# Kernel optimization log

Measured on AMD Instinct MI355X. Metric: run time of the kernel, lower is better.

The kernel has to match this reference:

```python
import jax, jax.numpy as jnp
import numpy as np

H = 1024
E = 8
TOP_K = 2
B, S = 4, 2048


def setup_inputs() -> dict:
    key = jax.random.key(0)
    ks = jax.random.split(key, 8)
    scale = 0.02
    return {
        "x": jax.random.normal(ks[0], (B, S, H), dtype=jnp.float32),
        "router_w": jax.random.normal(ks[1], (H, E), dtype=jnp.float32) * scale,
        "router_b": jnp.zeros((E,), dtype=jnp.float32),
        "w1": jax.random.normal(ks[2], (E, H, 4 * H), dtype=jnp.float32) * scale,
        "b1": jnp.zeros((E, 4 * H), dtype=jnp.float32),
        "w2": jax.random.normal(ks[3], (E, 4 * H, H), dtype=jnp.float32) * scale,
        "b2": jnp.zeros((E, H), dtype=jnp.float32),
    }


def reference(x, router_w, router_b, w1, b1, w2, b2):
    b, s, h = x.shape
    n_exp = w1.shape[0]
    x_flat = x.reshape(-1, h)  # [T, H]
    T = x_flat.shape[0]

    # Router: softmax then top-k, renormalize top-k probs (matches torch code).
    logits = x_flat @ router_w + router_b            # [T, E]
    probs = jax.nn.softmax(logits, axis=-1)
    top_values, top_indices = jax.lax.top_k(probs, TOP_K)  # [T, k]
    top_values = top_values / jnp.sum(top_values, axis=-1, keepdims=True)

    # Per-token combine weight for each expert (0 if token not routed there).
    combine = jnp.zeros((T, n_exp), dtype=x.dtype)
    combine = combine.at[jnp.arange(T)[:, None], top_indices].add(top_values)  # [T, E]

    # Loop over the small fixed expert set; masked combine weights zero out
    # contributions from unrouted tokens, matching the gather/scatter original.
    out = jnp.zeros_like(x_flat)
    for e in range(n_exp):
        hmid = jax.nn.gelu(x_flat @ w1[e] + b1[e], approximate=False)  # [T, 4H]
        y = hmid @ w2[e] + b2[e]                                       # [T, H]
        out = out + combine[:, e:e + 1] * y
    return out.reshape(b, s, h)
```

## Files before the change

kernel.cpp:

```cpp
#include <hip/hip_runtime.h>
#include <hip/hip_bf16.h>
#include <math.h>

#define TT 8192
#define HD 1024
#define FHD 4096
#define NE 8
#define NTMAX 136

typedef short s16x8 __attribute__((ext_vector_type(8)));
typedef float f32x4 __attribute__((ext_vector_type(4)));
using bf16 = __hip_bfloat16;
typedef unsigned int u32;

#define OFF_COUNTS 0
#define OFF_DONE   32
#define OFF_CURSOR 64
#define OFF_OFFS   128
#define OFF_E0     256
#define OFF_E1     (OFF_E0 + 4*TT)
#define OFF_W0     (OFF_E1 + 4*TT)
#define OFF_W1     (OFF_W0 + 4*TT)
#define OFF_S0     (OFF_W1 + 4*TT)
#define OFF_S1     (OFF_S0 + 4*TT)
#define OFF_TID    (OFF_S1 + 4*TT)
#define OFF_TW     (OFF_TID + 8*TT)
#define OFF_TMR    (OFF_TW + 8*TT)
#define OFF_TME    (OFF_TMR + 4*144)
#define OFF_TMN    (OFF_TME + 4*144)
#define OFF_XBF    (OFF_TMN + 64)
#define OFF_W1T    (OFF_XBF + 2*TT*HD)
#define OFF_W2T    (OFF_W1T + 2*NE*HD*FHD)
#define OFF_HMID   (OFF_W2T + 2*NE*HD*FHD)
#define OFF_YS     (OFF_HMID + (size_t)2*(2*TT)*FHD)

__device__ __forceinline__ void gload_lds16(const void* g, void* l) {
    __builtin_amdgcn_global_load_lds(
        (const __attribute__((address_space(1))) u32*)g,
        (__attribute__((address_space(3))) u32*)l, 16, 0, 0);
}

__global__ __launch_bounds__(256) void prep_kernel(
        const float* __restrict__ x, const float* __restrict__ rw, const float* __restrict__ rb,
        const float* __restrict__ w1, const float* __restrict__ w2,
        bf16* __restrict__ xbf, bf16* __restrict__ w1t, bf16* __restrict__ w2t,
        int* __restrict__ e0a, int* __restrict__ e1a,
        float* __restrict__ w0a, float* __restrict__ w1a,
        int* __restrict__ counts, int* __restrict__ done,
        int* __restrict__ offs, int* __restrict__ cursor,
        int* __restrict__ tmr, int* __restrict__ tme, int* __restrict__ tmn) {
    __shared__ float tile[64][65];
    __shared__ bf16 btile[64][264];
    int bid = blockIdx.x;
    int tid = threadIdx.x;
    if (bid < 4096) {
        const float* in; bf16* out; int R, C, rem;
        if (bid < 2048) { in = w1; out = w1t; R = HD;  C = FHD; rem = bid; }
        else            { in = w2; out = w2t; R = FHD; C = HD;  rem = bid - 2048; }
        int kch = R >> 8;
        int nch = C >> 6;
        int per = kch * nch;
        int e = rem / per;
        int rem2 = rem % per;
        int kc = rem2 / nch, nc = rem2 % nch;
        int k0 = kc << 8, n0 = nc << 6;
        const float* ine = in + (size_t)e * R * C;
        bf16* oute = out + (size_t)e * R * C;
        for (int s = 0; s < 4; ++s) {
            int ks = k0 + s * 64;
#pragma unroll
            for (int i = 0; i < 4; ++i) {
                int lin = tid + i * 256;
                int r = lin >> 4, cg = lin & 15;
                float4 v = *reinterpret_cast<const float4*>(&ine[(size_t)(ks + r) * C + n0 + cg * 4]);
                tile[r][cg * 4 + 0] = v.x; tile[r][cg * 4 + 1] = v.y;
                tile[r][cg * 4 + 2] = v.z; tile[r][cg * 4 + 3] = v.w;
            }
            __syncthreads();
#pragma unroll
            for (int i = 0; i < 4; ++i) {
                int lin = tid + i * 256;
                int n = lin >> 4, kg = lin & 15;
                bf16 h[4];
                h[0] = __float2bfloat16(tile[kg * 4 + 0][n]);
                h[1] = __float2bfloat16(tile[kg * 4 + 1][n]);
                h[2] = __float2bfloat16(tile[kg * 4 + 2][n]);
                h[3] = __float2bfloat16(tile[kg * 4 + 3][n]);
                *reinterpret_cast<uint2*>(&btile[n][s * 64 + kg * 4]) = *reinterpret_cast<uint2*>(h);
            }
            __syncthreads();
        }
#pragma unroll
        for (int i = 0; i < 8; ++i) {
            int lin = tid + i * 256;
            int n = lin >> 5, kk = lin & 31;
            *reinterpret_cast<uint4*>(&oute[(size_t)(n0 + n) * R + k0 + kk * 8]) =
                *reinterpret_cast<const uint4*>(&btile[n][kk * 8]);
        }
        return;
    }
    int rbid = bid - 4096;
    int wid = tid >> 6, lane = tid & 63;
    int t = rbid * 4 + wid;
    const float* xp = x + (size_t)t * HD + lane * 16;
    float xv[16];
#pragma unroll
    for (int j = 0; j < 4; ++j) {
        float4 v = *reinterpret_cast<const float4*>(&xp[j * 4]);
        xv[4 * j] = v.x; xv[4 * j + 1] = v.y; xv[4 * j + 2] = v.z; xv[4 * j + 3] = v.w;
    }
    {
        bf16 hv[16];
#pragma unroll
        for (int j = 0; j < 16; ++j) hv[j] = __float2bfloat16(xv[j]);
        uint4* dst = reinterpret_cast<uint4*>(&xbf[(size_t)t * HD + lane * 16]);
        dst[0] = reinterpret_cast<uint4*>(hv)[0];
        dst[1] = reinterpret_cast<uint4*>(hv)[1];
    }
    float acc[8] = {0.f, 0.f, 0.f, 0.f, 0.f, 0.f, 0.f, 0.f};
    const float* rp = rw + (size_t)(lane * 16) * NE;
#pragma unroll
    for (int hh = 0; hh < 16; ++hh) {
        float4 r0 = *reinterpret_cast<const float4*>(&rp[hh * 8]);
        float4 r1 = *reinterpret_cast<const float4*>(&rp[hh * 8 + 4]);
        acc[0] += xv[hh] * r0.x; acc[1] += xv[hh] * r0.y;
        acc[2] += xv[hh] * r0.z; acc[3] += xv[hh] * r0.w;
        acc[4] += xv[hh] * r1.x; acc[5] += xv[hh] * r1.y;
        acc[6] += xv[hh] * r1.z; acc[7] += xv[hh] * r1.w;
    }
#pragma unroll
    for (int e = 0; e < 8; ++e) {
#pragma unroll
        for (int off = 32; off > 0; off >>= 1) acc[e] += __shfl_xor(acc[e], off, 64);
    }
    if (lane == 0) {
        float lg[8];
#pragma unroll
        for (int e = 0; e < 8; ++e) lg[e] = acc[e] + rb[e];
        int a = 0;
#pragma unroll
        for (int e = 1; e < 8; ++e) if (lg[e] > lg[a]) a = e;
        int b = (a == 0) ? 1 : 0;
#pragma unroll
        for (int e = 0; e < 8; ++e) if (e != a && e != b && lg[e] > lg[b]) b = e;
        float wa = 1.0f / (1.0f + expf(lg[b] - lg[a]));
        float wb = 1.0f / (1.0f + expf(lg[a] - lg[b]));
        e0a[t] = a; e1a[t] = b; w0a[t] = wa; w1a[t] = wb;
        atomicAdd(&counts[a], 1);
        atomicAdd(&counts[b], 1);
    }
    __syncthreads();
    __shared__ int lastFlag;
    if (tid == 0) {
        __threadfence();
        lastFlag = (atomicAdd(done, 1) == 2047) ? 1 : 0;
    }
    __syncthreads();
    if (!lastFlag) return;
    __threadfence();
    __shared__ int cbase[NE + 1], tbase[NE + 1];
    if (tid == 0) {
        int s = 0, ntt = 0;
        for (int e = 0; e < NE; ++e) {
            int c = atomicAdd(&counts[e], 0);
            cbase[e] = s; tbase[e] = ntt;
            s += c; ntt += (c + 127) >> 7;
        }
        cbase[NE] = s; tbase[NE] = ntt;
        tmn[0] = ntt;
        offs[NE] = s;
    }
    __syncthreads();
    if (tid < NE) { offs[tid] = cbase[tid]; cursor[tid] = cbase[tid]; }
    if (tid < NTMAX) {
        int ntt = tbase[NE];
        if (tid < ntt) {
            int e = 0;
            while (tbase[e + 1] <= tid) ++e;
            tmr[tid] = cbase[e] + ((tid - tbase[e]) << 7);
            tme[tid] = e;
        } else { tmr[tid] = 0; tme[tid] = 0; }
    }
}

__global__ __launch_bounds__(256) void scatter_kernel(const int* __restrict__ e0a, const int* __restrict__ e1a,
        const float* __restrict__ w0a, const float* __restrict__ w1a,
        int* __restrict__ cursor, int* __restrict__ tid_arr, float* __restrict__ tw_arr,
        int* __restrict__ slot0, int* __restrict__ slot1) {
    int t = blockIdx.x * 256 + threadIdx.x;
    int s0 = atomicAdd(&cursor[e0a[t]], 1);
    tid_arr[s0] = t; tw_arr[s0] = w0a[t]; slot0[t] = s0;
    int s1 = atomicAdd(&cursor[e1a[t]], 1);
    tid_arr[s1] = t; tw_arr[s1] = w1a[t]; slot1[t] = s1;
}

__global__ __launch_bounds__(256) void gemm1_kernel(const bf16* __restrict__ xbf, const bf16* __restrict__ w1t,
        const float* __restrict__ b1, const int* __restrict__ offs,
        const int* __restrict__ tid_arr, bf16* __restrict__ hmid,
        const int* __restrict__ tmr, const int* __restrict__ tme, const int* __restrict__ tmn) {
    __shared__ bf16 As[128 * 32];
    __shared__ bf16 Bs[128 * 32];
    __shared__ int toks[128];
    int nwg = gridDim.x;
    int orig = blockIdx.x;
    int wg = (orig & 7) * (nwg >> 3) + (orig >> 3);
    int nt = wg / NTMAX;
    int tidx = wg % NTMAX;
    if (tidx >= tmn[0]) return;
    int e = tme[tidx];
    int row0 = tmr[tidx];
    int s1 = offs[e + 1];
    int n0 = nt * 128;
    int tid = threadIdx.x;
    if (tid < 128) { int s = row0 + tid; toks[tid] = tid_arr[(s < s1) ? s : (s1 - 1)]; }
    __syncthreads();
    int lane = tid & 63, w = tid >> 6;
    int wrow = (w >> 1) * 64, wcol = (w & 1) * 64;
    int lr = lane & 15, lk = (lane >> 4) * 8;
    int srow = lane >> 2, seg = lane & 3;
    int tokA0 = toks[w * 32 + srow];
    int tokA1 = toks[w * 32 + 16 + srow];
    const bf16* w1e = w1t + (size_t)e * FHD * HD;
    const bf16* bsrc0 = w1e + (size_t)(n0 + w * 32 + srow) * HD + seg * 8;
    const bf16* bsrc1 = w1e + (size_t)(n0 + w * 32 + 16 + srow) * HD + seg * 8;
    const bf16* asrc0 = xbf + (size_t)tokA0 * HD + seg * 8;
    const bf16* asrc1 = xbf + (size_t)tokA1 * HD + seg * 8;
    bf16* aDst0 = &As[(w * 32) * 32];
    bf16* aDst1 = &As[(w * 32 + 16) * 32];
    bf16* bDst0 = &Bs[(w * 32) * 32];
    bf16* bDst1 = &Bs[(w * 32 + 16) * 32];
    f32x4 acc[4][4] = {};
    for (int k0 = 0; k0 < HD; k0 += 32) {
        gload_lds16(asrc0 + k0, aDst0);
        gload_lds16(asrc1 + k0, aDst1);
        gload_lds16(bsrc0 + k0, bDst0);
        gload_lds16(bsrc1 + k0, bDst1);
        __syncthreads();
        s16x8 aF[4], bF[4];
#pragma unroll
        for (int m = 0; m < 4; ++m) aF[m] = *reinterpret_cast<const s16x8*>(&As[(wrow + m * 16 + lr) * 32 + lk]);
#pragma unroll
        for (int n = 0; n < 4; ++n) bF[n] = *reinterpret_cast<const s16x8*>(&Bs[(wcol + n * 16 + lr) * 32 + lk]);
#pragma unroll
        for (int m = 0; m < 4; ++m)
#pragma unroll
            for (int n = 0; n < 4; ++n)
                acc[m][n] = __builtin_amdgcn_mfma_f32_16x16x32_bf16(aF[m], bF[n], acc[m][n], 0, 0, 0);
        __syncthreads();
    }
#pragma unroll
    for (int m = 0; m < 4; ++m) {
#pragma unroll
        for (int n = 0; n < 4; ++n) {
            int col = n0 + wcol + n * 16 + lr;
            float bv = b1[(size_t)e * FHD + col];
#pragma unroll
            for (int r = 0; r < 4; ++r) {
                int row = wrow + m * 16 + (lane >> 4) * 4 + r;
                int slot = row0 + row;
                if (slot < s1) {
                    float v2 = acc[m][n][r] + bv;
                    v2 = 0.5f * v2 * (1.0f + erff(v2 * 0.70710678118f));
                    hmid[(size_t)slot * FHD + col] = __float2bfloat16(v2);
                }
            }
        }
    }
}

__global__ __launch_bounds__(256) void gemm2_kernel(const bf16* __restrict__ hmid, const bf16* __restrict__ w2t,
        const float* __restrict__ b2, const int* __restrict__ offs, float* __restrict__ ys,
        const int* __restrict__ tmr, const int* __restrict__ tme, const int* __restrict__ tmn) {
    __shared__ bf16 As[128 * 32];
    __shared__ bf16 Bs[128 * 32];
    int nwg = gridDim.x;
    int orig = blockIdx.x;
    int wg = (orig & 7) * (nwg >> 3) + (orig >> 3);
    int nt = wg / NTMAX;
    int tidx = wg % NTMAX;
    if (tidx >= tmn[0]) return;
    int e = tme[tidx];
    int row0 = tmr[tidx];
    int s1 = offs[e + 1];
    int n0 = nt * 128;
    int tid = threadIdx.x;
    int lane = tid & 63, w = tid >> 6;
    int wrow = (w >> 1) * 64, wcol = (w & 1) * 64;
    int lr = lane & 15, lk = (lane >> 4) * 8;
    int srow = lane >> 2, seg = lane & 3;
    int ar0 = row0 + w * 32 + srow;      if (ar0 >= s1) ar0 = s1 - 1;
    int ar1 = row0 + w * 32 + 16 + srow; if (ar1 >= s1) ar1 = s1 - 1;
    const bf16* w2e = w2t + (size_t)e * HD * FHD;
    const bf16* bsrc0 = w2e + (size_t)(n0 + w * 32 + srow) * FHD + seg * 8;
    const bf16* bsrc1 = w2e + (size_t)(n0 + w * 32 + 16 + srow) * FHD + seg * 8;
    const bf16* asrc0 = hmid + (size_t)ar0 * FHD + seg * 8;
    const bf16* asrc1 = hmid + (size_t)ar1 * FHD + seg * 8;
    bf16* aDst0 = &As[(w * 32) * 32];
    bf16* aDst1 = &As[(w * 32 + 16) * 32];
    bf16* bDst0 = &Bs[(w * 32) * 32];
    bf16* bDst1 = &Bs[(w * 32 + 16) * 32];
    f32x4 acc[4][4] = {};
    for (int k0 = 0; k0 < FHD; k0 += 32) {
        gload_lds16(asrc0 + k0, aDst0);
        gload_lds16(asrc1 + k0, aDst1);
        gload_lds16(bsrc0 + k0, bDst0);
        gload_lds16(bsrc1 + k0, bDst1);
        __syncthreads();
        s16x8 aF[4], bF[4];
#pragma unroll
        for (int m = 0; m < 4; ++m) aF[m] = *reinterpret_cast<const s16x8*>(&As[(wrow + m * 16 + lr) * 32 + lk]);
#pragma unroll
        for (int n = 0; n < 4; ++n) bF[n] = *reinterpret_cast<const s16x8*>(&Bs[(wcol + n * 16 + lr) * 32 + lk]);
#pragma unroll
        for (int m = 0; m < 4; ++m)
#pragma unroll
            for (int n = 0; n < 4; ++n)
                acc[m][n] = __builtin_amdgcn_mfma_f32_16x16x32_bf16(aF[m], bF[n], acc[m][n], 0, 0, 0);
        __syncthreads();
    }
#pragma unroll
    for (int m = 0; m < 4; ++m) {
#pragma unroll
        for (int n = 0; n < 4; ++n) {
            int col = n0 + wcol + n * 16 + lr;
            float bv = b2[(size_t)e * HD + col];
#pragma unroll
            for (int r = 0; r < 4; ++r) {
                int row = wrow + m * 16 + (lane >> 4) * 4 + r;
                int slot = row0 + row;
                if (slot < s1) ys[(size_t)slot * HD + col] = acc[m][n][r] + bv;
            }
        }
    }
}

__global__ __launch_bounds__(256) void combine_kernel(const float* __restrict__ ys,
        const int* __restrict__ slot0, const int* __restrict__ slot1,
        const float* __restrict__ tw, float* __restrict__ out) {
    int t = blockIdx.x;
    int c = threadIdx.x * 4;
    int sa = slot0[t], sb = slot1[t];
    float wa = tw[sa], wb = tw[sb];
    float4 a = *reinterpret_cast<const float4*>(&ys[(size_t)sa * HD + c]);
    float4 b = *reinterpret_cast<const float4*>(&ys[(size_t)sb * HD + c]);
    float4 o;
    o.x = wa * a.x + wb * b.x; o.y = wa * a.y + wb * b.y;
    o.z = wa * a.z + wb * b.z; o.w = wa * a.w + wb * b.w;
    *reinterpret_cast<float4*>(&out[(size_t)t * HD + c]) = o;
}

extern "C" void kernel_launch(void* const* d_in, const int* in_sizes, int n_in,
                              void* d_out, int out_size, void* d_ws, size_t ws_size,
                              hipStream_t stream) {
    const float* x  = (const float*)d_in[0];
    const float* rw = (const float*)d_in[1];
    const float* rb = (const float*)d_in[2];
    const float* w1 = (const float*)d_in[3];
    const float* b1 = (const float*)d_in[4];
    const float* w2 = (const float*)d_in[5];
    const float* b2 = (const float*)d_in[6];
    float* out = (float*)d_out;
    char* ws = (char*)d_ws;

    int*   counts  = (int*)(ws + OFF_COUNTS);
    int*   done    = (int*)(ws + OFF_DONE);
    int*   cursor  = (int*)(ws + OFF_CURSOR);
    int*   offs    = (int*)(ws + OFF_OFFS);
    int*   e0a     = (int*)(ws + OFF_E0);
    int*   e1a     = (int*)(ws + OFF_E1);
    float* w0a     = (float*)(ws + OFF_W0);
    float* w1a     = (float*)(ws + OFF_W1);
    int*   slot0   = (int*)(ws + OFF_S0);
    int*   slot1   = (int*)(ws + OFF_S1);
    int*   tid_arr = (int*)(ws + OFF_TID);
    float* tw_arr  = (float*)(ws + OFF_TW);
    int*   tmr     = (int*)(ws + OFF_TMR);
    int*   tme     = (int*)(ws + OFF_TME);
    int*   tmn     = (int*)(ws + OFF_TMN);
    bf16*  xbf     = (bf16*)(ws + OFF_XBF);
    bf16*  w1t     = (bf16*)(ws + OFF_W1T);
    bf16*  w2t     = (bf16*)(ws + OFF_W2T);
    bf16*  hmid    = (bf16*)(ws + OFF_HMID);
    float* ys      = (float*)(ws + OFF_YS);

    hipMemsetAsync(counts, 0, 64, stream);

    prep_kernel<<<6144, 256, 0, stream>>>(x, rw, rb, w1, w2, xbf, w1t, w2t,
        e0a, e1a, w0a, w1a, counts, done, offs, cursor, tmr, tme, tmn);
    scatter_kernel<<<TT / 256, 256, 0, stream>>>(e0a, e1a, w0a, w1a, cursor,
        tid_arr, tw_arr, slot0, slot1);
    gemm1_kernel<<<(FHD / 128) * NTMAX, 256, 0, stream>>>(xbf, w1t, b1, offs, tid_arr, hmid, tmr, tme, tmn);
    gemm2_kernel<<<(HD / 128) * NTMAX, 256, 0, stream>>>(hmid, w2t, b2, offs, ys, tmr, tme, tmn);
    combine_kernel<<<TT, 256, 0, stream>>>(ys, slot0, slot1, tw_arr, out);
}
```

Measured before the change: 917.2 us.

## Overlap w2 transpose with gemm1 by fusing both into one launch

The w2 fp32-to-bf16 transpose moves out of the prep kernel into the same grid as the first expert GEMM. Low block indices do the transpose panels and the rest run gemm1 tiles, so the bandwidth-bound conversion can overlap with the compute-bound GEMM. The fused kernel uses a shared 50KB LDS buffer for both roles, which may lower gemm1 occupancy compared with its original smaller footprint. Block dispatch order sends the transpose blocks first, which may delay the start of the GEMM work.

```diff
diff --git a/kernel.cpp b/kernel.cpp
--- a/kernel.cpp
+++ b/kernel.cpp
@@ -7,6 +7,7 @@
 #define FHD 4096
 #define NE 8
 #define NTMAX 136
+#define NWG1 4352
 
 typedef short s16x8 __attribute__((ext_vector_type(8)));
 typedef float f32x4 __attribute__((ext_vector_type(4)));
@@ -40,66 +41,67 @@
         (__attribute__((address_space(3))) u32*)l, 16, 0, 0);
 }
 
-__global__ __launch_bounds__(256) void prep_kernel(
+__device__ __forceinline__ void transpose_panel(const float* __restrict__ in,
+        bf16* __restrict__ out, int R, int C, int rem, int tid, char* smem) {
+    float (*tile)[65]  = reinterpret_cast<float(*)[65]>(smem);
+    bf16  (*btile)[264] = reinterpret_cast<bf16(*)[264]>(smem + 16640);
+    int kch = R >> 8, nch = C >> 6;
+    int per = kch * nch;
+    int e = rem / per;
+    int rem2 = rem % per;
+    int kc = rem2 / nch, nc = rem2 % nch;
+    int k0 = kc << 8, n0 = nc << 6;
+    const float* ine = in + (size_t)e * R * C;
+    bf16* oute = out + (size_t)e * R * C;
+    for (int s = 0; s < 4; ++s) {
+        int ks = k0 + s * 64;
+#pragma unroll
+        for (int i = 0; i < 4; ++i) {
+            int lin = tid + i * 256;
+            int r = lin >> 4, cg = lin & 15;
+            float4 v = *reinterpret_cast<const float4*>(&ine[(size_t)(ks + r) * C + n0 + cg * 4]);
+            tile[r][cg * 4 + 0] = v.x; tile[r][cg * 4 + 1] = v.y;
+            tile[r][cg * 4 + 2] = v.z; tile[r][cg * 4 + 3] = v.w;
+        }
+        __syncthreads();
+#pragma unroll
+        for (int i = 0; i < 4; ++i) {
+            int lin = tid + i * 256;
+            int n = lin >> 4, kg = lin & 15;
+            bf16 h[4];
+            h[0] = __float2bfloat16(tile[kg * 4 + 0][n]);
+            h[1] = __float2bfloat16(tile[kg * 4 + 1][n]);
+            h[2] = __float2bfloat16(tile[kg * 4 + 2][n]);
+            h[3] = __float2bfloat16(tile[kg * 4 + 3][n]);
+            *reinterpret_cast<uint2*>(&btile[n][s * 64 + kg * 4]) = *reinterpret_cast<uint2*>(h);
+        }
+        __syncthreads();
+    }
+#pragma unroll
+    for (int i = 0; i < 8; ++i) {
+        int lin = tid + i * 256;
+        int n = lin >> 5, kk = lin & 31;
+        *reinterpret_cast<uint4*>(&oute[(size_t)(n0 + n) * R + k0 + kk * 8]) =
+            *reinterpret_cast<const uint4*>(&btile[n][kk * 8]);
+    }
+}
+
+__global__ __launch_bounds__(256) void fused1_kernel(
         const float* __restrict__ x, const float* __restrict__ rw, const float* __restrict__ rb,
-        const float* __restrict__ w1, const float* __restrict__ w2,
-        bf16* __restrict__ xbf, bf16* __restrict__ w1t, bf16* __restrict__ w2t,
+        const float* __restrict__ w1, bf16* __restrict__ xbf, bf16* __restrict__ w1t,
         int* __restrict__ e0a, int* __restrict__ e1a,
         float* __restrict__ w0a, float* __restrict__ w1a,
         int* __restrict__ counts, int* __restrict__ done,
         int* __restrict__ offs, int* __restrict__ cursor,
         int* __restrict__ tmr, int* __restrict__ tme, int* __restrict__ tmn) {
-    __shared__ float tile[64][65];
-    __shared__ bf16 btile[64][264];
+    __shared__ __attribute__((aligned(16))) char smem[50432];
     int bid = blockIdx.x;
     int tid = threadIdx.x;
-    if (bid < 4096) {
-        const float* in; bf16* out; int R, C, rem;
-        if (bid < 2048) { in = w1; out = w1t; R = HD;  C = FHD; rem = bid; }
-        else            { in = w2; out = w2t; R = FHD; C = HD;  rem = bid - 2048; }
-        int kch = R >> 8;
-        int nch = C >> 6;
-        int per = kch * nch;
-        int e = rem / per;
-        int rem2 = rem % per;
-        int kc = rem2 / nch, nc = rem2 % nch;
-        int k0 = kc << 8, n0 = nc << 6;
-        const float* ine = in + (size_t)e * R * C;
-        bf16* oute = out + (size_t)e * R * C;
-        for (int s = 0; s < 4; ++s) {
-            int ks = k0 + s * 64;
-#pragma unroll
-            for (int i = 0; i < 4; ++i) {
-                int lin = tid + i * 256;
-                int r = lin >> 4, cg = lin & 15;
-                float4 v = *reinterpret_cast<const float4*>(&ine[(size_t)(ks + r) * C + n0 + cg * 4]);
-                tile[r][cg * 4 + 0] = v.x; tile[r][cg * 4 + 1] = v.y;
-                tile[r][cg * 4 + 2] = v.z; tile[r][cg * 4 + 3] = v.w;
-            }
-            __syncthreads();
-#pragma unroll
-            for (int i = 0; i < 4; ++i) {
-                int lin = tid + i * 256;
-                int n = lin >> 4, kg = lin & 15;
-                bf16 h[4];
-                h[0] = __float2bfloat16(tile[kg * 4 + 0][n]);
-                h[1] = __float2bfloat16(tile[kg * 4 + 1][n]);
-                h[2] = __float2bfloat16(tile[kg * 4 + 2][n]);
-                h[3] = __float2bfloat16(tile[kg * 4 + 3][n]);
-                *reinterpret_cast<uint2*>(&btile[n][s * 64 + kg * 4]) = *reinterpret_cast<uint2*>(h);
-            }
-            __syncthreads();
-        }
-#pragma unroll
-        for (int i = 0; i < 8; ++i) {
-            int lin = tid + i * 256;
-            int n = lin >> 5, kk = lin & 31;
-            *reinterpret_cast<uint4*>(&oute[(size_t)(n0 + n) * R + k0 + kk * 8]) =
-                *reinterpret_cast<const uint4*>(&btile[n][kk * 8]);
-        }
+    if (bid < 2048) {
+        transpose_panel(w1, w1t, HD, FHD, bid, tid, smem);
         return;
     }
-    int rbid = bid - 4096;
+    int rbid = bid - 2048;
     int wid = tid >> 6, lane = tid & 63;
     int t = rbid * 4 + wid;
     const float* xp = x + (size_t)t * HD + lane * 16;
@@ -194,16 +196,24 @@
     tid_arr[s1] = t; tw_arr[s1] = w1a[t]; slot1[t] = s1;
 }
 
-__global__ __launch_bounds__(256) void gemm1_kernel(const bf16* __restrict__ xbf, const bf16* __restrict__ w1t,
+__global__ __launch_bounds__(256) void fused2_kernel(
+        const float* __restrict__ w2, bf16* __restrict__ w2t,
+        const bf16* __restrict__ xbf, const bf16* __restrict__ w1t,
         const float* __restrict__ b1, const int* __restrict__ offs,
         const int* __restrict__ tid_arr, bf16* __restrict__ hmid,
         const int* __restrict__ tmr, const int* __restrict__ tme, const int* __restrict__ tmn) {
-    __shared__ bf16 As[128 * 32];
-    __shared__ bf16 Bs[128 * 32];
-    __shared__ int toks[128];
-    int nwg = gridDim.x;
-    int orig = blockIdx.x;
-    int wg = (orig & 7) * (nwg >> 3) + (orig >> 3);
+    __shared__ __attribute__((aligned(16))) char smem[50432];
+    int bid = blockIdx.x;
+    int tid = threadIdx.x;
+    if (bid < 2048) {
+        transpose_panel(w2, w2t, FHD, HD, bid, tid, smem);
+        return;
+    }
+    bf16* As = reinterpret_cast<bf16*>(smem);
+    bf16* Bs = reinterpret_cast<bf16*>(smem + 8192);
+    int*  toks = reinterpret_cast<int*>(smem + 16384);
+    int orig = bid - 2048;
+    int wg = (orig & 7) * (NWG1 >> 3) + (orig >> 3);
     int nt = wg / NTMAX;
     int tidx = wg % NTMAX;
     if (tidx >= tmn[0]) return;
@@ -211,7 +221,6 @@
     int row0 = tmr[tidx];
     int s1 = offs[e + 1];
     int n0 = nt * 128;
-    int tid = threadIdx.x;
     if (tid < 128) { int s = row0 + tid; toks[tid] = tid_arr[(s < s1) ? s : (s1 - 1)]; }
     __syncthreads();
     int lane = tid & 63, w = tid >> 6;
@@ -385,11 +394,12 @@
 
     hipMemsetAsync(counts, 0, 64, stream);
 
-    prep_kernel<<<6144, 256, 0, stream>>>(x, rw, rb, w1, w2, xbf, w1t, w2t,
+    fused1_kernel<<<4096, 256, 0, stream>>>(x, rw, rb, w1, xbf, w1t,
         e0a, e1a, w0a, w1a, counts, done, offs, cursor, tmr, tme, tmn);
     scatter_kernel<<<TT / 256, 256, 0, stream>>>(e0a, e1a, w0a, w1a, cursor,
         tid_arr, tw_arr, slot0, slot1);
-    gemm1_kernel<<<(FHD / 128) * NTMAX, 256, 0, stream>>>(xbf, w1t, b1, offs, tid_arr, hmid, tmr, tme, tmn);
+    fused2_kernel<<<2048 + NWG1, 256, 0, stream>>>(w2, w2t, xbf, w1t, b1, offs,
+        tid_arr, hmid, tmr, tme, tmn);
     gemm2_kernel<<<(HD / 128) * NTMAX, 256, 0, stream>>>(hmid, w2t, b2, offs, ys, tmr, tme, tmn);
     combine_kernel<<<TT, 256, 0, stream>>>(ys, slot0, slot1, tw_arr, out);
 }
```

Result: no change. 917.8 us (+0.1%).
